# Kernel tuning notes

Hardware: AMD Instinct MI355X
Metric: run time of the kernel (lower is better)

Reference implementation:

```python
import jax, jax.numpy as jnp
import numpy as np

NEGPOS_RATIO = 3


def _smooth_l1(pred, tgt):
    d = jnp.abs(pred - tgt)
    return jnp.where(d < 1.0, 0.5 * d * d, d - 0.5)


def setup_inputs() -> dict:
    key = jax.random.key(0)
    B, P, C = 64, 8732, 81
    ks = jax.random.split(key, 7)
    loc_dataT = jax.random.normal(ks[0], (B, P, 4), jnp.float32)
    conf_dataT = jax.random.normal(ks[1], (B, P, C), jnp.float32)
    loc_dataS = jax.random.normal(ks[2], (B, P, 4), jnp.float32)
    conf_dataS = jax.random.normal(ks[3], (B, P, C), jnp.float32)
    loc_t = jax.random.normal(ks[4], (B, P, 4), jnp.float32)
    is_pos = jax.random.uniform(ks[5], (B, P)) < 0.02
    labels = jax.random.randint(ks[6], (B, P), 1, C, dtype=jnp.int32)
    conf_t = jnp.where(is_pos, labels, 0).astype(jnp.int32)
    return {
        "loc_dataT": loc_dataT, "conf_dataT": conf_dataT,
        "loc_dataS": loc_dataS, "conf_dataS": conf_dataS,
        "loc_t": loc_t, "conf_t": conf_t,
    }


def _multibox_losses(loc_dataT, conf_dataT, loc_dataS, conf_dataS, loc_t, conf_t):
    B, P, C = conf_dataT.shape
    pos = conf_t > 0                                    # [B,P]
    posf = pos.astype(conf_dataT.dtype)

    # Localization SmoothL1 over positive priors (reduction='sum')
    loss_lT = jnp.sum(_smooth_l1(loc_dataT, loc_t) * posf[..., None])
    loss_lS = jnp.sum(_smooth_l1(loc_dataS, loc_t) * posf[..., None])

    # Per-prior CE loss: logsumexp(conf) - conf[gt]  (== -log_softmax[gt])
    def per_prior_ce(conf):
        lse = jax.nn.logsumexp(conf, axis=-1)           # [B,P]
        gt = jnp.take_along_axis(conf, conf_t[..., None].astype(jnp.int32), axis=-1)[..., 0]
        return lse - gt

    lcT = per_prior_ce(conf_dataT)                      # [B,P]
    lcS = per_prior_ce(conf_dataS)

    # Hard negative mining: rank negatives by loss (positives zeroed first)
    def neg_mask(lc, num_neg):
        lc_m = jnp.where(pos, 0.0, lc)
        order = jnp.argsort(-lc_m, axis=1)              # descending sort indices
        rank = jnp.argsort(order, axis=1)               # rank of each prior
        return rank < num_neg

    num_pos = jnp.sum(pos.astype(jnp.int32), axis=1, keepdims=True)   # [B,1]
    num_neg = jnp.minimum(NEGPOS_RATIO * num_pos, P - 1)
    negT = neg_mask(lcT, num_neg)
    negS = neg_mask(lcS, num_neg)

    # Confidence CE over positives + mined negatives (reduction='sum')
    loss_cT = jnp.sum(jnp.where(pos | negT, lcT, 0.0))
    loss_cS = jnp.sum(jnp.where(pos | negS, lcS, 0.0))

    N = jnp.sum(num_pos).astype(conf_dataT.dtype)
    return jnp.stack([loss_lT / N, loss_cT / N, loss_lS / N, loss_cS / N])


def reference(loc_dataT, conf_dataT, loc_dataS, conf_dataS, loc_t, conf_t):
    # Teacher branch is detached in the original module.
    loc_dataT = jax.lax.stop_gradient(loc_dataT)
    conf_dataT = jax.lax.stop_gradient(conf_dataT)
    return _multibox_losses(loc_dataT, conf_dataT, loc_dataS, conf_dataS, loc_t, conf_t)
```

## Files before the change

### kernel.cpp

```cpp
#include <hip/hip_runtime.h>

#define BB 64
#define PP 8732
#define CC 81
#define RPB 128
#define SLOTS ((RPB * CC) / 4)
#define TPB 512


__device__ __forceinline__ float sl1(float d) {
    d = fabsf(d);
    return d < 1.0f ? 0.5f * d * d : d - 0.5f;
}

__device__ __forceinline__ float blockReduceF(float v, volatile float* sb) {
    for (int off = 32; off; off >>= 1) v += __shfl_xor(v, off, 64);
    __syncthreads();
    if ((threadIdx.x & 63) == 0) sb[threadIdx.x >> 6] = v;
    __syncthreads();
    float r = 0.0f;
    int nw = blockDim.x >> 6;
    for (int i = 0; i < nw; ++i) r += sb[i];
    return r;
}

__device__ __forceinline__ int blockReduceI(int v, volatile int* sb) {
    for (int off = 32; off; off >>= 1) v += __shfl_xor(v, off, 64);
    __syncthreads();
    if ((threadIdx.x & 63) == 0) sb[threadIdx.x >> 6] = v;
    __syncthreads();
    int r = 0;
    int nw = blockDim.x >> 6;
    for (int i = 0; i < nw; ++i) r += sb[i];
    return r;
}

__global__ void kInit(float* acc, int* numpos, int* ctr) {
    int t = threadIdx.x;
    if (t < 4) acc[t] = 0.0f;
    if (t < BB) numpos[t] = 0;
    if (t == 0) ctr[0] = 0;
}

__device__ __forceinline__ void processSlot(int i, float4 v,
                                            float* psum, float* spill) {
    int f = i << 2;
    int r0 = f / 81;
    int rem = f - r0 * 81;
    float e0 = __expf(v.x), e1 = __expf(v.y), e2 = __expf(v.z), e3 = __expf(v.w);
    float t01 = e0 + e1;
    float tot = t01 + e2 + e3;
    float ps = tot;
    if (rem >= 78) {
        int ns = 81 - rem;
        float a = (ns == 1) ? e0 : ((ns == 2) ? t01 : t01 + e2);
        ps = a;
        spill[r0 + 1] = tot - a;
    }
    psum[i] = ps;
}

__device__ __forceinline__ void phase2(float* __restrict__ dst, size_t rowBase,
                                       int nrows, int tid,
                                       const float* psum, const float* spill,
                                       const float* gtval, const int* gtraw) {
    int r = tid >> 1, h = tid & 1;
    if (r < nrows) {
        int i0 = (81 * r + 3) >> 2;
        int i1 = (81 * (r + 1) + 3) >> 2;
        int mid = (i0 + i1 + 1) >> 1;
        int lo = h ? mid : i0;
        int hi = h ? i1 : mid;
        float s = (h == 0 && (r & 3)) ? spill[r] : 0.0f;
        for (int i = lo; i < hi; ++i) s += psum[i];
        s += __shfl_xor(s, 1, 64);
        if (h == 0) {
            float lc = __logf(s) - gtval[r];
            dst[rowBase + r] = (gtraw[r] > 0) ? -(lc + 1.0f) : lc;
        }
    }
}

__global__ __launch_bounds__(TPB, 6) void kMain(
        const float* __restrict__ confT, const float* __restrict__ confS,
        const int* __restrict__ conft,
        const float4* __restrict__ locT4, const float4* __restrict__ locS4,
        const float4* __restrict__ loct4,
        float* __restrict__ lcT, float* __restrict__ lcS,
        float* acc, int* numpos) {
    __shared__ float psum[SLOTS];
    __shared__ float spill[RPB];
    __shared__ float gtval[RPB];
    __shared__ int gtraw[RPB];
    __shared__ float fsb[TPB / 64];
    __shared__ int isb[TPB / 64];

    int b = blockIdx.y;
    int p0 = blockIdx.x * RPB;
    int nrows = min(RPB, PP - p0);
    int tid = threadIdx.x;
    size_t rowBase = (size_t)b * PP + p0;
    const float* __restrict__ rowT = confT + rowBase * CC;
    const float* __restrict__ rowS = confS + rowBase * CC;
    const float4* __restrict__ gT = (const float4*)rowT;
    const float4* __restrict__ gS = (const float4*)rowS;

    bool hasrow = tid < nrows;
    int g_ = 0;
    if (hasrow) g_ = conft[rowBase + tid];

    float sT = 0.0f, sS = 0.0f;
    int cnt = 0;

    if (nrows == RPB) {
        float4 v[5];
        #pragma unroll
        for (int k = 0; k < 5; ++k) v[k] = gT[tid + TPB * k];
        float4 vx;
        bool extra = tid < (SLOTS - 5 * TPB);
        if (extra) vx = gT[5 * TPB + tid];
        float gtvT = 0.0f, gtvS = 0.0f;
        if (hasrow) {
            gtvT = rowT[tid * CC + g_];
            gtvS = rowS[tid * CC + g_];
            if (g_ > 0) {
                size_t idx = rowBase + tid;
                float4 gt = loct4[idx];
                float4 aT = locT4[idx];
                float4 aS = locS4[idx];
                sT = sl1(aT.x - gt.x) + sl1(aT.y - gt.y) + sl1(aT.z - gt.z) + sl1(aT.w - gt.w);
                sS = sl1(aS.x - gt.x) + sl1(aS.y - gt.y) + sl1(aS.z - gt.z) + sl1(aS.w - gt.w);
                cnt = 1;
            }
        }
        #pragma unroll
        for (int k = 0; k < 5; ++k) processSlot(tid + TPB * k, v[k], psum, spill);
        if (extra) processSlot(5 * TPB + tid, vx, psum, spill);
        float4 w[5];
        #pragma unroll
        for (int k = 0; k < 5; ++k) w[k] = gS[tid + TPB * k];
        float4 wx;
        if (extra) wx = gS[5 * TPB + tid];
        if (hasrow) { gtraw[tid] = g_; gtval[tid] = gtvT; }
        __syncthreads();
        phase2(lcT, rowBase, nrows, tid, psum, spill, gtval, gtraw);
        __syncthreads();
        #pragma unroll
        for (int k = 0; k < 5; ++k) processSlot(tid + TPB * k, w[k], psum, spill);
        if (extra) processSlot(5 * TPB + tid, wx, psum, spill);
        if (hasrow) gtval[tid] = gtvS;
        __syncthreads();
        phase2(lcS, rowBase, nrows, tid, psum, spill, gtval, gtraw);
    } else {
        int nq = (nrows * CC) >> 2;
        float gtvT = 0.0f, gtvS = 0.0f;
        if (hasrow) {
            gtvT = rowT[tid * CC + g_];
            gtvS = rowS[tid * CC + g_];
            if (g_ > 0) {
                size_t idx = rowBase + tid;
                float4 gt = loct4[idx];
                float4 aT = locT4[idx];
                float4 aS = locS4[idx];
                sT = sl1(aT.x - gt.x) + sl1(aT.y - gt.y) + sl1(aT.z - gt.z) + sl1(aT.w - gt.w);
                sS = sl1(aS.x - gt.x) + sl1(aS.y - gt.y) + sl1(aS.z - gt.z) + sl1(aS.w - gt.w);
                cnt = 1;
            }
        }
        for (int i = tid; i < nq; i += TPB) processSlot(i, gT[i], psum, spill);
        if (hasrow) { gtraw[tid] = g_; gtval[tid] = gtvT; }
        __syncthreads();
        phase2(lcT, rowBase, nrows, tid, psum, spill, gtval, gtraw);
        __syncthreads();
        for (int i = tid; i < nq; i += TPB) processSlot(i, gS[i], psum, spill);
        if (hasrow) gtval[tid] = gtvS;
        __syncthreads();
        phase2(lcS, rowBase, nrows, tid, psum, spill, gtval, gtraw);
    }

    sT = blockReduceF(sT, fsb);
    sS = blockReduceF(sS, fsb);
    cnt = blockReduceI(cnt, isb);
    if (tid == 0) {
        if (sT != 0.0f) atomicAdd(&acc[0], sT);
        if (sS != 0.0f) atomicAdd(&acc[1], sS);
        if (cnt) atomicAdd(&numpos[b], cnt);
    }
}

__global__ __launch_bounds__(1024) void kC(const float* __restrict__ lcT,
                                           const float* __restrict__ lcS,
                                           const int* __restrict__ numpos,
                                           float* acc, int* ctr,
                                           float* __restrict__ out) {
    __shared__ unsigned keys[PP];
    __shared__ int whist[16 * 256];
    __shared__ int hist[256];
    __shared__ float fsb[16];
    __shared__ int isb[16];
    __shared__ int selBin, selAbove, lastFlag;
    int b = blockIdx.y;
    int tid = threadIdx.x;
    const float* src = ((blockIdx.x == 0) ? lcT : lcS) + (size_t)b * PP;

    float posSum = 0.0f;
    for (int i = tid; i < PP; i += 1024) {
        float v = src[i];
        keys[i] = (v < 0.0f) ? 0u : __float_as_uint(v);
        if (v < 0.0f) posSum += (-v - 1.0f);
    }
    posSum = blockReduceF(posSum, fsb);

    int np = numpos[b];
    int k = min(3 * np, PP - 1);
    float mined = 0.0f;
    if (k > 0) {
        unsigned prefix = 0;
        int kk = k;
        int wid = tid >> 6;
        for (int round = 0; round < 4; ++round) {
            int shift = 24 - 8 * round;
            for (int i = tid; i < 16 * 256; i += 1024) whist[i] = 0;
            __syncthreads();
            for (int i = tid; i < PP; i += 1024) {
                unsigned key = keys[i];
                bool match = (round == 0) || ((key >> (shift + 8)) == prefix);
                if (match) atomicAdd(&whist[(wid << 8) | ((key >> shift) & 0xFF)], 1);
            }
            __syncthreads();
            if (tid < 256) {
                int h2 = 0;
                #pragma unroll
                for (int w = 0; w < 16; ++w) h2 += whist[(w << 8) | tid];
                hist[tid] = h2;
            }
            __syncthreads();
            for (int d = 1; d < 256; d <<= 1) {
                int v2 = 0;
                if (tid < 256) v2 = hist[tid] + ((tid + d < 256) ? hist[tid + d] : 0);
                __syncthreads();
                if (tid < 256) hist[tid] = v2;
                __syncthreads();
            }
            if (tid < 256) {
                int above = (tid < 255) ? hist[tid + 1] : 0;
                if (above < kk && hist[tid] >= kk) {
                    selBin = tid;
                    selAbove = above;
                }
            }
            __syncthreads();
            prefix = (prefix << 8) | (unsigned)selBin;
            kk -= selAbove;
            __syncthreads();
        }
        int c = 0;
        float s = 0.0f;
        for (int i = tid; i < PP; i += 1024) {
            unsigned key = keys[i];
            if (key > prefix) { c += 1; s += __uint_as_float(key); }
        }
        c = blockReduceI(c, isb);
        s = blockReduceF(s, fsb);
        mined = s + (float)(k - c) * __uint_as_float(prefix);
    }
    if (tid == 0) {
        atomicAdd(&acc[(blockIdx.x == 0) ? 2 : 3], posSum + mined);
        __threadfence();
        int old = atomicAdd(ctr, 1);
        lastFlag = (old == 2 * BB - 1) ? 1 : 0;
    }
    __syncthreads();
    if (lastFlag) {
        __threadfence();
        int v = 0;
        if (tid < BB)
            v = __hip_atomic_load(&numpos[tid], __ATOMIC_RELAXED, __HIP_MEMORY_SCOPE_AGENT);
        if (tid < 64)
            for (int off = 32; off; off >>= 1) v += __shfl_xor(v, off, 64);
        if (tid == 0) {
            float N = (float)v;
            float a0 = __hip_atomic_load(&acc[0], __ATOMIC_RELAXED, __HIP_MEMORY_SCOPE_AGENT);
            float a1 = __hip_atomic_load(&acc[1], __ATOMIC_RELAXED, __HIP_MEMORY_SCOPE_AGENT);
            float a2 = __hip_atomic_load(&acc[2], __ATOMIC_RELAXED, __HIP_MEMORY_SCOPE_AGENT);
            float a3 = __hip_atomic_load(&acc[3], __ATOMIC_RELAXED, __HIP_MEMORY_SCOPE_AGENT);
            out[0] = a0 / N;
            out[1] = a2 / N;
            out[2] = a1 / N;
            out[3] = a3 / N;
        }
    }
}

extern "C" void kernel_launch(void* const* d_in, const int* in_sizes, int n_in,
                              void* d_out, int out_size, void* d_ws, size_t ws_size,
                              hipStream_t stream) {
    const float* locT  = (const float*)d_in[0];
    const float* confT = (const float*)d_in[1];
    const float* locS  = (const float*)d_in[2];
    const float* confS = (const float*)d_in[3];
    const float* loct  = (const float*)d_in[4];
    const int*   conft = (const int*)d_in[5];
    float* out = (float*)d_out;

    float* lcT = (float*)d_ws;
    float* lcS = lcT + (size_t)BB * PP;
    float* acc = lcS + (size_t)BB * PP;
    int* numpos = (int*)(acc + 4);
    int* ctr = numpos + BB;

    kInit<<<1, 64, 0, stream>>>(acc, numpos, ctr);

    dim3 gM((PP + RPB - 1) / RPB, BB);
    kMain<<<gM, TPB, 0, stream>>>(confT, confS, conft,
                                  (const float4*)locT, (const float4*)locS,
                                  (const float4*)loct, lcT, lcS, acc, numpos);

    dim3 gC(2, BB);
    kC<<<gC, 1024, 0, stream>>>(lcT, lcS, numpos, acc, ctr, out);
}
```

Before: 440.4 us.

## Restructure CE pass into per-wavefront row tiles split over teacher/student grid

The main streaming kernel now gives each 64-lane wavefront 16 rows with its own LDS slice, so there are no block-wide barriers. A grid z dimension separates the teacher and student confidence tensors, which creates more, smaller blocks for better occupancy and latency hiding. Localization partial sums are accumulated per batch, and the top-k kernel's suffix scan now uses wave shuffles instead of a barrier-heavy LDS scan. The trade-off is more blocks, duplicate conf_t loads, and more atomics per batch.

```diff
diff --git a/kernel.cpp b/kernel.cpp
--- a/kernel.cpp
+++ b/kernel.cpp
@@ -3,9 +3,11 @@
 #define BB 64
 #define PP 8732
 #define CC 81
-#define RPB 128
-#define SLOTS ((RPB * CC) / 4)
-#define TPB 512
+#define RPW 16
+#define WSLOTS ((RPW * CC) / 4)
+#define WSTRIDE (WSLOTS + RPW)
+#define WPB 4
+#define ROWS_PB (RPW * WPB)
 
 
 __device__ __forceinline__ float sl1(float d) {
@@ -35,10 +37,10 @@
     return r;
 }
 
-__global__ void kInit(float* acc, int* numpos, int* ctr) {
+__global__ void kInit(float* acc, int* numpos, int* ctr, float* locPart) {
     int t = threadIdx.x;
     if (t < 4) acc[t] = 0.0f;
-    if (t < BB) numpos[t] = 0;
+    if (t < BB) { numpos[t] = 0; locPart[t] = 0.0f; locPart[BB + t] = 0.0f; }
     if (t == 0) ctr[0] = 0;
 }
 
@@ -60,137 +62,108 @@
     psum[i] = ps;
 }
 
-__device__ __forceinline__ void phase2(float* __restrict__ dst, size_t rowBase,
-                                       int nrows, int tid,
-                                       const float* psum, const float* spill,
-                                       const float* gtval, const int* gtraw) {
-    int r = tid >> 1, h = tid & 1;
-    if (r < nrows) {
-        int i0 = (81 * r + 3) >> 2;
-        int i1 = (81 * (r + 1) + 3) >> 2;
-        int mid = (i0 + i1 + 1) >> 1;
-        int lo = h ? mid : i0;
-        int hi = h ? i1 : mid;
-        float s = (h == 0 && (r & 3)) ? spill[r] : 0.0f;
-        for (int i = lo; i < hi; ++i) s += psum[i];
-        s += __shfl_xor(s, 1, 64);
-        if (h == 0) {
-            float lc = __logf(s) - gtval[r];
-            dst[rowBase + r] = (gtraw[r] > 0) ? -(lc + 1.0f) : lc;
-        }
-    }
-}
-
-__global__ __launch_bounds__(TPB, 6) void kMain(
+__global__ __launch_bounds__(256, 8) void kStream(
         const float* __restrict__ confT, const float* __restrict__ confS,
         const int* __restrict__ conft,
         const float4* __restrict__ locT4, const float4* __restrict__ locS4,
         const float4* __restrict__ loct4,
         float* __restrict__ lcT, float* __restrict__ lcS,
-        float* acc, int* numpos) {
-    __shared__ float psum[SLOTS];
-    __shared__ float spill[RPB];
-    __shared__ float gtval[RPB];
-    __shared__ int gtraw[RPB];
-    __shared__ float fsb[TPB / 64];
-    __shared__ int isb[TPB / 64];
-
+        float* __restrict__ locPart, int* __restrict__ numpos) {
+    __shared__ float lds[WPB * WSTRIDE];
     int b = blockIdx.y;
-    int p0 = blockIdx.x * RPB;
-    int nrows = min(RPB, PP - p0);
+    int z = blockIdx.z;
     int tid = threadIdx.x;
-    size_t rowBase = (size_t)b * PP + p0;
-    const float* __restrict__ rowT = confT + rowBase * CC;
-    const float* __restrict__ rowS = confS + rowBase * CC;
-    const float4* __restrict__ gT = (const float4*)rowT;
-    const float4* __restrict__ gS = (const float4*)rowS;
-
-    bool hasrow = tid < nrows;
-    int g_ = 0;
-    if (hasrow) g_ = conft[rowBase + tid];
+    int w = tid >> 6, lane = tid & 63;
+    int row0 = blockIdx.x * ROWS_PB + w * RPW;
+    int nr = min(RPW, PP - row0);
+    const float* __restrict__ conf = z ? confS : confT;
+    float* __restrict__ dst = z ? lcS : lcT;
+    float* psum = lds + w * WSTRIDE;
+    float* spill = psum + WSLOTS;
 
     float sT = 0.0f, sS = 0.0f;
     int cnt = 0;
-
-    if (nrows == RPB) {
-        float4 v[5];
-        #pragma unroll
-        for (int k = 0; k < 5; ++k) v[k] = gT[tid + TPB * k];
-        float4 vx;
-        bool extra = tid < (SLOTS - 5 * TPB);
-        if (extra) vx = gT[5 * TPB + tid];
-        float gtvT = 0.0f, gtvS = 0.0f;
-        if (hasrow) {
-            gtvT = rowT[tid * CC + g_];
-            gtvS = rowS[tid * CC + g_];
-            if (g_ > 0) {
-                size_t idx = rowBase + tid;
-                float4 gt = loct4[idx];
-                float4 aT = locT4[idx];
-                float4 aS = locS4[idx];
-                sT = sl1(aT.x - gt.x) + sl1(aT.y - gt.y) + sl1(aT.z - gt.z) + sl1(aT.w - gt.w);
-                sS = sl1(aS.x - gt.x) + sl1(aS.y - gt.y) + sl1(aS.z - gt.z) + sl1(aS.w - gt.w);
-                cnt = 1;
-            }
-        }
-        #pragma unroll
-        for (int k = 0; k < 5; ++k) processSlot(tid + TPB * k, v[k], psum, spill);
-        if (extra) processSlot(5 * TPB + tid, vx, psum, spill);
-        float4 w[5];
-        #pragma unroll
-        for (int k = 0; k < 5; ++k) w[k] = gS[tid + TPB * k];
-        float4 wx;
-        if (extra) wx = gS[5 * TPB + tid];
-        if (hasrow) { gtraw[tid] = g_; gtval[tid] = gtvT; }
-        __syncthreads();
-        phase2(lcT, rowBase, nrows, tid, psum, spill, gtval, gtraw);
-        __syncthreads();
-        #pragma unroll
-        for (int k = 0; k < 5; ++k) processSlot(tid + TPB * k, w[k], psum, spill);
-        if (extra) processSlot(5 * TPB + tid, wx, psum, spill);
-        if (hasrow) gtval[tid] = gtvS;
-        __syncthreads();
-        phase2(lcS, rowBase, nrows, tid, psum, spill, gtval, gtraw);
-    } else {
-        int nq = (nrows * CC) >> 2;
-        float gtvT = 0.0f, gtvS = 0.0f;
-        if (hasrow) {
-            gtvT = rowT[tid * CC + g_];
-            gtvS = rowS[tid * CC + g_];
-            if (g_ > 0) {
-                size_t idx = rowBase + tid;
-                float4 gt = loct4[idx];
-                float4 aT = locT4[idx];
-                float4 aS = locS4[idx];
-                sT = sl1(aT.x - gt.x) + sl1(aT.y - gt.y) + sl1(aT.z - gt.z) + sl1(aT.w - gt.w);
-                sS = sl1(aS.x - gt.x) + sl1(aS.y - gt.y) + sl1(aS.z - gt.z) + sl1(aS.w - gt.w);
-                cnt = 1;
-            }
-        }
-        for (int i = tid; i < nq; i += TPB) processSlot(i, gT[i], psum, spill);
-        if (hasrow) { gtraw[tid] = g_; gtval[tid] = gtvT; }
-        __syncthreads();
-        phase2(lcT, rowBase, nrows, tid, psum, spill, gtval, gtraw);
-        __syncthreads();
-        for (int i = tid; i < nq; i += TPB) processSlot(i, gS[i], psum, spill);
-        if (hasrow) gtval[tid] = gtvS;
-        __syncthreads();
-        phase2(lcS, rowBase, nrows, tid, psum, spill, gtval, gtraw);
-    }
-
-    sT = blockReduceF(sT, fsb);
-    sS = blockReduceF(sS, fsb);
-    cnt = blockReduceI(cnt, isb);
-    if (tid == 0) {
-        if (sT != 0.0f) atomicAdd(&acc[0], sT);
-        if (sS != 0.0f) atomicAdd(&acc[1], sS);
-        if (cnt) atomicAdd(&numpos[b], cnt);
+    int g_ = 0;
+
+    if (nr > 0) {
+        size_t rowBase = (size_t)b * PP + row0;
+        const float* __restrict__ rowp = conf + rowBase * (size_t)CC;
+        const float4* __restrict__ g4 = (const float4*)rowp;
+        bool hasrow = lane < nr;
+        if (hasrow) g_ = conft[rowBase + lane];
+        float gtv = 0.0f;
+
+        if (nr == RPW) {
+            float4 v0 = g4[lane];
+            float4 v1 = g4[lane + 64];
+            float4 v2 = g4[lane + 128];
+            float4 v3 = g4[lane + 192];
+            float4 v4 = g4[lane + 256];
+            float4 vx;
+            bool extra = lane < (WSLOTS - 320);
+            if (extra) vx = g4[320 + lane];
+            if (hasrow) gtv = rowp[lane * CC + g_];
+            processSlot(lane,       v0, psum, spill);
+            processSlot(lane + 64,  v1, psum, spill);
+            processSlot(lane + 128, v2, psum, spill);
+            processSlot(lane + 192, v3, psum, spill);
+            processSlot(lane + 256, v4, psum, spill);
+            if (extra) processSlot(320 + lane, vx, psum, spill);
+        } else {
+            int nq = (nr * CC) >> 2;
+            for (int i = lane; i < nq; i += 64)
+                processSlot(i, g4[i], psum, spill);
+            if (hasrow) gtv = rowp[lane * CC + g_];
+        }
+
+        if (z == 0 && hasrow && g_ > 0) {
+            size_t idx = rowBase + lane;
+            float4 gt = loct4[idx];
+            float4 aT = locT4[idx];
+            float4 aS = locS4[idx];
+            sT = sl1(aT.x - gt.x) + sl1(aT.y - gt.y) + sl1(aT.z - gt.z) + sl1(aT.w - gt.w);
+            sS = sl1(aS.x - gt.x) + sl1(aS.y - gt.y) + sl1(aS.z - gt.z) + sl1(aS.w - gt.w);
+            cnt = 1;
+        }
+
+        asm volatile("s_waitcnt lgkmcnt(0)" ::: "memory");
+        __builtin_amdgcn_sched_barrier(0);
+
+        int r = lane >> 2, h = lane & 3;
+        float gv = __shfl(gtv, r, 64);
+        int   gr = __shfl(g_,  r, 64);
+        if (r < nr) {
+            int i0 = (81 * r + 3) >> 2;
+            int i1 = (81 * (r + 1) + 3) >> 2;
+            float s = (h == 0 && (r & 3)) ? spill[r] : 0.0f;
+            for (int i = i0 + h; i < i1; i += 4) s += psum[i];
+            s += __shfl_xor(s, 1, 64);
+            s += __shfl_xor(s, 2, 64);
+            if (h == 0) {
+                float lc = __logf(s) - gv;
+                dst[rowBase + r] = (gr > 0) ? -(lc + 1.0f) : lc;
+            }
+        }
+    }
+
+    if (z == 0) {
+        for (int off = 32; off; off >>= 1) {
+            sT  += __shfl_xor(sT,  off, 64);
+            sS  += __shfl_xor(sS,  off, 64);
+            cnt += __shfl_xor(cnt, off, 64);
+        }
+        if (lane == 0 && cnt) {
+            atomicAdd(&locPart[b], sT);
+            atomicAdd(&locPart[BB + b], sS);
+            atomicAdd(&numpos[b], cnt);
+        }
     }
 }
 
 __global__ __launch_bounds__(1024) void kC(const float* __restrict__ lcT,
                                            const float* __restrict__ lcS,
                                            const int* __restrict__ numpos,
+                                           const float* __restrict__ locPart,
                                            float* acc, int* ctr,
                                            float* __restrict__ out) {
     __shared__ unsigned keys[PP];
@@ -198,9 +171,10 @@
     __shared__ int hist[256];
     __shared__ float fsb[16];
     __shared__ int isb[16];
-    __shared__ int selBin, selAbove, lastFlag;
+    __shared__ int selBin, selAbove, lastFlag, wsum[4];
     int b = blockIdx.y;
     int tid = threadIdx.x;
+    int lane = tid & 63;
     const float* src = ((blockIdx.x == 0) ? lcT : lcS) + (size_t)b * PP;
 
     float posSum = 0.0f;
@@ -235,13 +209,23 @@
                 hist[tid] = h2;
             }
             __syncthreads();
-            for (int d = 1; d < 256; d <<= 1) {
-                int v2 = 0;
-                if (tid < 256) v2 = hist[tid] + ((tid + d < 256) ? hist[tid + d] : 0);
-                __syncthreads();
-                if (tid < 256) hist[tid] = v2;
-                __syncthreads();
-            }
+            int x = (tid < 256) ? hist[tid] : 0;
+            for (int d = 1; d < 64; d <<= 1) {
+                int y = __shfl_down(x, d, 64);
+                if (lane + d < 64) x += y;
+            }
+            if (tid < 256 && lane == 0) wsum[tid >> 6] = x;
+            __syncthreads();
+            if (tid < 256) {
+                int wv = tid >> 6;
+                int add = 0;
+                if (wv < 3) add += wsum[wv + 1];
+                if (wv < 2) add += wsum[wv + 2];
+                if (wv < 1) add += wsum[wv + 3];
+                int sfx = x + add;
+                hist[tid] = sfx;
+            }
+            __syncthreads();
             if (tid < 256) {
                 int above = (tid < 255) ? hist[tid + 1] : 0;
                 if (above < kk && hist[tid] >= kk) {
@@ -274,19 +258,26 @@
     if (lastFlag) {
         __threadfence();
         int v = 0;
-        if (tid < BB)
-            v = __hip_atomic_load(&numpos[tid], __ATOMIC_RELAXED, __HIP_MEMORY_SCOPE_AGENT);
-        if (tid < 64)
-            for (int off = 32; off; off >>= 1) v += __shfl_xor(v, off, 64);
+        float pT = 0.0f, pS = 0.0f;
+        if (tid < BB) {
+            v  = __hip_atomic_load(&numpos[tid], __ATOMIC_RELAXED, __HIP_MEMORY_SCOPE_AGENT);
+            pT = __hip_atomic_load(&locPart[tid], __ATOMIC_RELAXED, __HIP_MEMORY_SCOPE_AGENT);
+            pS = __hip_atomic_load(&locPart[BB + tid], __ATOMIC_RELAXED, __HIP_MEMORY_SCOPE_AGENT);
+        }
+        if (tid < 64) {
+            for (int off = 32; off; off >>= 1) {
+                v  += __shfl_xor(v,  off, 64);
+                pT += __shfl_xor(pT, off, 64);
+                pS += __shfl_xor(pS, off, 64);
+            }
+        }
         if (tid == 0) {
             float N = (float)v;
-            float a0 = __hip_atomic_load(&acc[0], __ATOMIC_RELAXED, __HIP_MEMORY_SCOPE_AGENT);
-            float a1 = __hip_atomic_load(&acc[1], __ATOMIC_RELAXED, __HIP_MEMORY_SCOPE_AGENT);
             float a2 = __hip_atomic_load(&acc[2], __ATOMIC_RELAXED, __HIP_MEMORY_SCOPE_AGENT);
             float a3 = __hip_atomic_load(&acc[3], __ATOMIC_RELAXED, __HIP_MEMORY_SCOPE_AGENT);
-            out[0] = a0 / N;
+            out[0] = pT / N;
             out[1] = a2 / N;
-            out[2] = a1 / N;
+            out[2] = pS / N;
             out[3] = a3 / N;
         }
     }
@@ -308,14 +299,16 @@
     float* acc = lcS + (size_t)BB * PP;
     int* numpos = (int*)(acc + 4);
     int* ctr = numpos + BB;
-
-    kInit<<<1, 64, 0, stream>>>(acc, numpos, ctr);
-
-    dim3 gM((PP + RPB - 1) / RPB, BB);
-    kMain<<<gM, TPB, 0, stream>>>(confT, confS, conft,
-                                  (const float4*)locT, (const float4*)locS,
-                                  (const float4*)loct, lcT, lcS, acc, numpos);
+    float* locPart = (float*)(ctr + 1);
+
+    kInit<<<1, 64, 0, stream>>>(acc, numpos, ctr, locPart);
+
+    dim3 gS((PP + ROWS_PB - 1) / ROWS_PB, BB, 2);
+    kStream<<<gS, 256, 0, stream>>>(confT, confS, conft,
+                                    (const float4*)locT, (const float4*)locS,
+                                    (const float4*)loct, lcT, lcS,
+                                    locPart, numpos);
 
     dim3 gC(2, BB);
-    kC<<<gC, 1024, 0, stream>>>(lcT, lcS, numpos, acc, ctr, out);
-}
+    kC<<<gC, 1024, 0, stream>>>(lcT, lcS, numpos, locPart, acc, ctr, out);
+}
```

Result: faster. 425.4 us (-3.4%).
